# Kernel tuning notes

Measured on AMD Instinct MI355X. Metric: run time of the kernel, lower is better.

Reference implementation:

```python
import jax, jax.numpy as jnp
import numpy as np

B, S, D = 4, 2048, 1024
H = 16
HD = D // H  # 64
ROPE_BASE = 10000.0


def _rope_cache(seq_len, dim, dtype=jnp.float32):
    inv_freq = 1.0 / (ROPE_BASE ** (jnp.arange(0, dim, 2, dtype=jnp.float32) / dim))
    t = jnp.arange(seq_len, dtype=jnp.float32)
    freqs = jnp.outer(t, inv_freq)            # [S, dim/2]
    emb = jnp.concatenate([freqs, freqs], -1)  # [S, dim]
    return jnp.cos(emb).astype(dtype), jnp.sin(emb).astype(dtype)


def _rotate_half(x):
    x1, x2 = jnp.split(x, 2, axis=-1)
    return jnp.concatenate([-x2, x1], axis=-1)


def setup_inputs() -> dict:
    key = jax.random.key(0)
    k1, k2, k3 = jax.random.split(key, 3)
    x = jax.random.normal(k1, (B, S, D), dtype=jnp.float32)
    attention_mask = jnp.ones((B, S), dtype=jnp.int32)
    # torch nn.Linear weight is [out, in]; we store [in, out] for x @ W
    w_qkv = jax.random.normal(k2, (D, 3 * D), dtype=jnp.float32) * (1.0 / np.sqrt(D))
    w_out = jax.random.normal(k3, (D, D), dtype=jnp.float32) * (1.0 / np.sqrt(D))
    return {"x": x, "attention_mask": attention_mask, "w_qkv": w_qkv, "w_out": w_out}


def reference(x, attention_mask, w_qkv, w_out):
    b, s, d = x.shape
    qkv = x @ w_qkv                                  # [B,S,3D]
    qkv = qkv.reshape(b, s, 3, H, HD)
    q, k, v = [jnp.transpose(qkv[:, :, i], (0, 2, 1, 3)) for i in range(3)]  # [B,H,S,HD]
    cos, sin = _rope_cache(s, HD, x.dtype)           # [S,HD]
    cos = cos[None, None]                            # [1,1,S,HD]
    sin = sin[None, None]
    q = q * cos + _rotate_half(q) * sin
    k = k * cos + _rotate_half(k) * sin
    scale = 1.0 / np.sqrt(HD)
    scores = jnp.einsum("bhqd,bhkd->bhqk", q, k) * scale  # [B,H,S,S]
    causal = jnp.triu(jnp.ones((s, s), dtype=bool), k=1)
    neg_inf = jnp.finfo(scores.dtype).min
    scores = jnp.where(causal[None, None], -jnp.inf, scores)
    pad = (attention_mask == 0)[:, None, None, :]    # [B,1,1,S]
    scores = jnp.where(pad, -jnp.inf, scores)
    attn = jax.nn.softmax(scores, axis=-1)
    out = jnp.einsum("bhqk,bhkd->bhqd", attn, v)     # [B,H,S,HD]
    out = jnp.transpose(out, (0, 2, 1, 3)).reshape(b, s, d)
    return out @ w_out
```

## Files before the change

### kernel.cpp

```cpp
#include <hip/hip_runtime.h>

#define BQ 4
#define SQ 2048
#define DQ 1024
#define HQ 16
#define BHQ 64

typedef __attribute__((ext_vector_type(8))) short short8;
typedef __attribute__((ext_vector_type(4))) float f32x4;
typedef __attribute__((ext_vector_type(16))) float f32x16;
typedef __attribute__((ext_vector_type(2))) unsigned int u32x2;
typedef unsigned short u16;
typedef unsigned int u32;
typedef unsigned long long u64;

__device__ __forceinline__ u16 f2bf(float f) {
  u32 u = __float_as_uint(f);
  u32 r = u + 0x7fffu + ((u >> 16) & 1u);
  return (u16)(r >> 16);
}
__device__ __forceinline__ float bf2f(u16 h) {
  return __uint_as_float(((u32)h) << 16);
}

__device__ __forceinline__ u32 pkbf(float lo, float hi_) {
  u32 r;
  asm("v_cvt_pk_bf16_f32 %0, %1, %2" : "=v"(r) : "v"(lo), "v"(hi_));
  return r;
}
__device__ __forceinline__ float fexp2(float x) {
  float r;
  asm("v_exp_f32 %0, %1" : "=v"(r) : "v"(x));
  return r;
}
__device__ __forceinline__ float xmax32(float x) { return fmaxf(x, __shfl_xor(x, 32)); }
__device__ __forceinline__ float xsum32(float x) { return x + __shfl_xor(x, 32); }
__device__ __forceinline__ u32 xword(u32 send) { return (u32)__shfl_xor((int)send, 32); }

__device__ __forceinline__ void gload_lds16(const void* g, void* l) {
  __builtin_amdgcn_global_load_lds(
      (const __attribute__((address_space(1))) u32*)(unsigned long long)g,
      (__attribute__((address_space(3))) u32*)(u32)(unsigned long long)l,
      16, 0, 0);
}

__global__ __launch_bounds__(256) void k_cvt(const float* __restrict__ in, u16* __restrict__ out, int n4) {
  int i = blockIdx.x * 256 + threadIdx.x;
  if (i < n4) {
    float4 v = ((const float4*)in)[i];
    ushort4 o;
    o.x = f2bf(v.x); o.y = f2bf(v.y); o.z = f2bf(v.z); o.w = f2bf(v.w);
    ((ushort4*)out)[i] = o;
  }
}

__global__ __launch_bounds__(256) void k_transpose_cvt(const float* __restrict__ in, u16* __restrict__ out,
                                                       int R, int C) {
  __shared__ float t[32][33];
  int c0 = blockIdx.x * 32, r0 = blockIdx.y * 32;
  int tx = threadIdx.x & 31, ty = threadIdx.x >> 5;
  for (int rr = ty; rr < 32; rr += 8)
    t[rr][tx] = in[(size_t)(r0 + rr) * C + c0 + tx];
  __syncthreads();
  for (int rr = ty; rr < 32; rr += 8)
    out[(size_t)(c0 + rr) * R + r0 + tx] = f2bf(t[tx][rr]);
}

__global__ __launch_bounds__(256) void k_rope_table(float* __restrict__ tab) {
  int i = blockIdx.x * 256 + threadIdx.x;
  if (i >= SQ * 32) return;
  int s = i >> 5, dp = i & 31;
  float invf = expf(-0.28782313662425576f * (float)dp);
  float ang = (float)s * invf;
  tab[i * 2] = cosf(ang);
  tab[i * 2 + 1] = sinf(ang);
}

__global__ __launch_bounds__(256) void k_mflags(const int* __restrict__ mask, u64* __restrict__ mbits) {
  int tid = threadIdx.x;
  int b = tid >> 6, c = tid & 63;
  int all1 = 1;
  for (int i = 0; i < 32; ++i) all1 &= (mask[b * SQ + c * 32 + i] != 0) ? 1 : 0;
  u64 m = __ballot(all1);
  if (c == 0) mbits[b] = m;
}

template <int EPI>
__global__ __launch_bounds__(256) void k_gemm(const u16* __restrict__ A, const u16* __restrict__ Bt,
                                              float* __restrict__ Cf, u16* __restrict__ qb,
                                              u16* __restrict__ kb, u16* __restrict__ vTs,
                                              const float* __restrict__ tab, int K) {
  __shared__ u16 lA[128 * 64];
  __shared__ u16 lB[128 * 64];
  int tid = threadIdx.x, w = tid >> 6, l = tid & 63;
  int wm = w >> 1, wn = w & 1;
  int tm = blockIdx.x, tn = blockIdx.y;
  int li = l & 15, lg = l >> 4;
  const u16* gA = A + (size_t)tm * 128 * K;
  const u16* gB = Bt + (size_t)tn * 128 * K;
  f32x4 acc[4][4];
#pragma unroll
  for (int i = 0; i < 4; i++)
#pragma unroll
    for (int j = 0; j < 4; j++) acc[i][j] = (f32x4){0.f, 0.f, 0.f, 0.f};

  int lr = l >> 3, lslot = l & 7;
  int scol = ((lslot ^ lr) * 8);

  for (int kt = 0; kt < K; kt += 64) {
    __syncthreads();
#pragma unroll
    for (int i = 0; i < 4; ++i) {
      int ch = i * 4 + w;
      int row = ch * 8 + lr;
      gload_lds16(gA + (size_t)row * K + kt + scol, &lA[ch * 512]);
      gload_lds16(gB + (size_t)row * K + kt + scol, &lB[ch * 512]);
    }
    __syncthreads();
#pragma unroll
    for (int kk = 0; kk < 2; ++kk) {
      short8 af[4], bfr[4];
#pragma unroll
      for (int mf = 0; mf < 4; ++mf) {
        int row = wm * 64 + mf * 16 + li;
        af[mf] = *(const short8*)&lA[row * 64 + (((kk * 4 + lg)) ^ (row & 7)) * 8];
      }
#pragma unroll
      for (int nf = 0; nf < 4; ++nf) {
        int row = wn * 64 + nf * 16 + li;
        bfr[nf] = *(const short8*)&lB[row * 64 + (((kk * 4 + lg)) ^ (row & 7)) * 8];
      }
#pragma unroll
      for (int mf = 0; mf < 4; ++mf)
#pragma unroll
        for (int nf = 0; nf < 4; ++nf)
          acc[mf][nf] = __builtin_amdgcn_mfma_f32_16x16x32_bf16(af[mf], bfr[nf], acc[mf][nf], 0, 0, 0);
    }
  }
  if (EPI == 0) {
#pragma unroll
    for (int mf = 0; mf < 4; ++mf) {
      int mg0 = tm * 128 + wm * 64 + mf * 16 + lg * 4;
#pragma unroll
      for (int nf = 0; nf < 4; ++nf) {
        int ng = tn * 128 + wn * 64 + nf * 16 + li;
#pragma unroll
        for (int r = 0; r < 4; ++r)
          Cf[(size_t)(mg0 + r) * 1024 + ng] = acc[mf][nf][r];
      }
    }
  } else {
    int which = tn >> 3;
    int h = (tn & 7) * 2 + wn;
    int b = tm >> 4;
    if (which < 2) {
      float scale = (which == 0) ? 0.125f * 1.44269504088896f : 1.0f;
      u16* qk = (which == 0 ? qb : kb) + (((size_t)b * HQ + h) * SQ << 6);
#pragma unroll
      for (int mf = 0; mf < 4; ++mf) {
#pragma unroll
        for (int r = 0; r < 4; ++r) {
          int s = (tm * 128 + wm * 64 + mf * 16 + lg * 4 + r) & 2047;
          u16* dst = qk + ((size_t)s << 6);
#pragma unroll
          for (int nf2 = 0; nf2 < 2; ++nf2) {
            int dp = nf2 * 16 + li;
            float2 cs = *(const float2*)&tab[(s * 32 + dp) * 2];
            float a = acc[mf][nf2][r];
            float bb = acc[mf][nf2 + 2][r];
            dst[dp] = f2bf((a * cs.x - bb * cs.y) * scale);
            dst[dp + 32] = f2bf((bb * cs.x + a * cs.y) * scale);
          }
        }
      }
    } else {
#pragma unroll
      for (int mf = 0; mf < 4; ++mf) {
        int s0 = (tm * 128 + wm * 64 + mf * 16 + lg * 4) & 2047;
        int kt = s0 >> 5, kk0 = s0 & 31;
        int slot = kk0 >> 3;
        size_t tb = (((size_t)(b * HQ + h) * 64 + kt) * 64);
#pragma unroll
        for (int nf = 0; nf < 4; ++nf) {
          int d = nf * 16 + li;
          u32 w0 = pkbf(acc[mf][nf][0], acc[mf][nf][1]);
          u32 w1 = pkbf(acc[mf][nf][2], acc[mf][nf][3]);
          size_t off = (tb + d) * 32 + ((slot ^ ((d >> 1) & 3)) << 3) + (kk0 & 7);
          *(u32x2*)&vTs[off] = (u32x2){w0, w1};
        }
      }
    }
  }
}

__global__ __launch_bounds__(256) void k_flash7(const u16* __restrict__ Q, const u16* __restrict__ Kb,
                                                const u16* __restrict__ VTs, const int* __restrict__ mask,
                                                const u64* __restrict__ mbits, u16* __restrict__ O) {
  __shared__ alignas(16) u16 Kl[2][2048];
  __shared__ alignas(16) u16 Vl[2][2048];
  int bid = blockIdx.x;
  int bh = bid & 63;
  int u = bid >> 6, v = u & 3, k4 = u >> 2;
  int qsup = (k4 == 0) ? v : (k4 == 1) ? 7 - v : (k4 == 2) ? 8 + v : 15 - v;
  int tid = threadIdx.x, w = tid >> 6, l = tid & 63;
  int j = l & 31, hi = l >> 5;
  int myqt = qsup * 4 + w;
  int nt = qsup * 4 + 4;
  int b = bh >> 4, h = bh & 15;
  const int* mp = mask + b * SQ + 4 * hi;
  u64 mb = mbits[b];

  int sr = tid >> 3, sc16 = tid & 7;
  const u16* Kg0 = Kb + ((size_t)bh * SQ) * 64 + sr * 64 + ((sc16 ^ (sr & 7)) * 8);
  const u16* Vg0 = VTs + ((size_t)bh * 64) * 2048 + tid * 8;
  u16* KlB = &Kl[0][(size_t)w * 512];
  u16* VlB = &Vl[0][(size_t)w * 512];

  int qbase = myqt * 32;
  const u16* qp = Q + ((size_t)bh * SQ + qbase + j) * 64 + hi * 8;
  short8 qf[4];
#pragma unroll
  for (int kb = 0; kb < 4; ++kb) qf[kb] = *(const short8*)(qp + kb * 16);

  f32x16 o0, o1;
#pragma unroll
  for (int i = 0; i < 16; ++i) { o0[i] = 0.f; o1[i] = 0.f; }
  float mrun = -INFINITY, lrun = 0.f;

  int swK = (j & 7), swV = (j >> 1) & 3;

  gload_lds16(Kg0, KlB);
  gload_lds16(Vg0, VlB);
  __syncthreads();

  for (int kt = 0; kt < nt; ++kt) {
    int cur = kt & 1;
    if (kt + 1 < nt) {
      gload_lds16(Kg0 + (size_t)(kt + 1) * 2048, KlB + (cur ^ 1) * 2048);
      gload_lds16(Vg0 + (size_t)(kt + 1) * 2048, VlB + (cur ^ 1) * 2048);
    }

    if (kt <= myqt) {
      const u16* Kc = Kl[cur];
      const u16* Vc = Vl[cur];

      short8 kcf[4];
#pragma unroll
      for (int kb = 0; kb < 4; ++kb)
        kcf[kb] = *(const short8*)&Kc[j * 64 + (((hi + 2 * kb)) ^ swK) * 8];

      f32x16 s;
#pragma unroll
      for (int i = 0; i < 16; ++i) s[i] = 0.f;
      __builtin_amdgcn_s_setprio(1);
#pragma unroll
      for (int kb = 0; kb < 4; ++kb)
        s = __builtin_amdgcn_mfma_f32_32x32x16_bf16(kcf[kb], qf[kb], s, 0, 0, 0);
      __builtin_amdgcn_s_setprio(0);

      short8 va0 = *(const short8*)&Vc[j * 32 + ((hi) ^ swV) * 8];
      short8 va1 = *(const short8*)&Vc[j * 32 + ((hi + 2) ^ swV) * 8];
      short8 vb0 = *(const short8*)&Vc[(j + 32) * 32 + ((hi) ^ swV) * 8];
      short8 vb1 = *(const short8*)&Vc[(j + 32) * 32 + ((hi + 2) ^ swV) * 8];

      if (!((mb >> kt) & 1ull)) {
#pragma unroll
        for (int rq = 0; rq < 4; ++rq) {
          int4 mv = *(const int4*)(mp + kt * 32 + 8 * rq);
          if (!mv.x) s[4 * rq + 0] = -INFINITY;
          if (!mv.y) s[4 * rq + 1] = -INFINITY;
          if (!mv.z) s[4 * rq + 2] = -INFINITY;
          if (!mv.w) s[4 * rq + 3] = -INFINITY;
        }
      }
      if (kt == myqt) {
#pragma unroll
        for (int rq = 0; rq < 4; ++rq)
#pragma unroll
          for (int t = 0; t < 4; ++t)
            if (8 * rq + 4 * hi + t > j) s[4 * rq + t] = -INFINITY;
      }

      float t0 = fmaxf(fmaxf(fmaxf(s[0], s[1]), fmaxf(s[2], s[3])),
                       fmaxf(fmaxf(s[4], s[5]), fmaxf(s[6], s[7])));
      t0 = fmaxf(t0, fmaxf(fmaxf(fmaxf(s[8], s[9]), fmaxf(s[10], s[11])),
                           fmaxf(fmaxf(s[12], s[13]), fmaxf(s[14], s[15]))));
      if (!__all(t0 <= mrun + 8.0f)) {
        float tm2 = xmax32(t0);
        float mn = fmaxf(fmaxf(mrun, tm2), -1e30f);
        float alpha = fexp2(mrun - mn);
        mrun = mn;
        lrun *= alpha;
#pragma unroll
        for (int i = 0; i < 16; ++i) { o0[i] *= alpha; o1[i] *= alpha; }
      }
      float ts = 0.f;
#pragma unroll
      for (int i = 0; i < 16; ++i) {
        float pv = fexp2(s[i] - mrun);
        s[i] = pv;
        ts += pv;
      }
      lrun += ts;

      u32 pa[4], pb[4];
#pragma unroll
      for (int q2 = 0; q2 < 4; ++q2) {
        pa[q2] = pkbf(s[4 * q2 + 0], s[4 * q2 + 1]);
        pb[q2] = pkbf(s[4 * q2 + 2], s[4 * q2 + 3]);
      }
      u32 ya01 = xword(hi ? pa[0] : pa[1]);
      u32 yb01 = xword(hi ? pb[0] : pb[1]);
      u32 ya23 = xword(hi ? pa[2] : pa[3]);
      u32 yb23 = xword(hi ? pb[2] : pb[3]);
      union { short8 s8; u32 wd[4]; } f0, f1;
      f0.wd[0] = hi ? ya01 : pa[0];
      f0.wd[1] = hi ? yb01 : pb[0];
      f0.wd[2] = hi ? pa[1] : ya01;
      f0.wd[3] = hi ? pb[1] : yb01;
      f1.wd[0] = hi ? ya23 : pa[2];
      f1.wd[1] = hi ? yb23 : pb[2];
      f1.wd[2] = hi ? pa[3] : ya23;
      f1.wd[3] = hi ? pb[3] : yb23;

      __builtin_amdgcn_s_setprio(1);
      o0 = __builtin_amdgcn_mfma_f32_32x32x16_bf16(va0, f0.s8, o0, 0, 0, 0);
      o0 = __builtin_amdgcn_mfma_f32_32x32x16_bf16(va1, f1.s8, o0, 0, 0, 0);
      o1 = __builtin_amdgcn_mfma_f32_32x32x16_bf16(vb0, f0.s8, o1, 0, 0, 0);
      o1 = __builtin_amdgcn_mfma_f32_32x32x16_bf16(vb1, f1.s8, o1, 0, 0, 0);
      __builtin_amdgcn_s_setprio(0);
    }

    __syncthreads();
  }

  float lfull = xsum32(lrun);
  float inv = 1.0f / lfull;
  u16* ob = O + ((size_t)b * SQ + qbase + j) * DQ + h * 64 + 4 * hi;
#pragma unroll
  for (int q2 = 0; q2 < 4; ++q2) {
#pragma unroll
    for (int e = 0; e < 2; ++e) {
      *(u32*)(ob + 8 * q2 + 2 * e) = pkbf(o0[4 * q2 + 2 * e] * inv, o0[4 * q2 + 2 * e + 1] * inv);
      *(u32*)(ob + 32 + 8 * q2 + 2 * e) = pkbf(o1[4 * q2 + 2 * e] * inv, o1[4 * q2 + 2 * e + 1] * inv);
    }
  }
}

extern "C" void kernel_launch(void* const* d_in, const int* in_sizes, int n_in,
                              void* d_out, int out_size, void* d_ws, size_t ws_size,
                              hipStream_t stream) {
  const float* x = (const float*)d_in[0];
  const int* mask = (const int*)d_in[1];
  const float* wqkv = (const float*)d_in[2];
  const float* wout = (const float*)d_in[3];
  float* out = (float*)d_out;
  char* ws = (char*)d_ws;

  u16* xb    = (u16*)(ws + 0);
  u16* wqkvT = (u16*)(ws + 16777216);
  u16* woutT = (u16*)(ws + 23068672);
  u16* qbuf  = (u16*)(ws + 25165824);
  u16* kbuf  = (u16*)(ws + 41943040);
  u16* vTs   = (u16*)(ws + 75497472);
  u16* attnb = (u16*)(ws + 92274688);
  float* tab = (float*)(ws + 109051904);
  u64* mbits = (u64*)(ws + 109576192);

  k_rope_table<<<256, 256, 0, stream>>>(tab);
  k_mflags<<<1, 256, 0, stream>>>(mask, mbits);
  k_cvt<<<8192, 256, 0, stream>>>(x, xb, 2097152);
  k_transpose_cvt<<<dim3(96, 32), 256, 0, stream>>>(wqkv, wqkvT, 1024, 3072);
  k_transpose_cvt<<<dim3(32, 32), 256, 0, stream>>>(wout, woutT, 1024, 1024);
  k_gemm<1><<<dim3(64, 24), 256, 0, stream>>>(xb, wqkvT, nullptr, qbuf, kbuf, vTs, tab, 1024);
  k_flash7<<<1024, 256, 0, stream>>>(qbuf, kbuf, vTs, mask, mbits, attnb);
  k_gemm<0><<<dim3(64, 8), 256, 0, stream>>>(attnb, woutT, out, nullptr, nullptr, nullptr, nullptr, 1024);
}
```

Measured before the change: 198.2 us.

## Fuse preprocessing kernels into one launch and swizzle GEMM block mapping for XCD locality

```diff
diff --git a/kernel.cpp b/kernel.cpp
--- a/kernel.cpp
+++ b/kernel.cpp
@@ -44,21 +44,11 @@
       16, 0, 0);
 }
 
-__global__ __launch_bounds__(256) void k_cvt(const float* __restrict__ in, u16* __restrict__ out, int n4) {
-  int i = blockIdx.x * 256 + threadIdx.x;
-  if (i < n4) {
-    float4 v = ((const float4*)in)[i];
-    ushort4 o;
-    o.x = f2bf(v.x); o.y = f2bf(v.y); o.z = f2bf(v.z); o.w = f2bf(v.w);
-    ((ushort4*)out)[i] = o;
-  }
-}
-
-__global__ __launch_bounds__(256) void k_transpose_cvt(const float* __restrict__ in, u16* __restrict__ out,
-                                                       int R, int C) {
+__device__ __forceinline__ void transpose_body(const float* __restrict__ in, u16* __restrict__ out,
+                                               int R, int C, int bx, int by, int tid) {
   __shared__ float t[32][33];
-  int c0 = blockIdx.x * 32, r0 = blockIdx.y * 32;
-  int tx = threadIdx.x & 31, ty = threadIdx.x >> 5;
+  int c0 = bx * 32, r0 = by * 32;
+  int tx = tid & 31, ty = tid >> 5;
   for (int rr = ty; rr < 32; rr += 8)
     t[rr][tx] = in[(size_t)(r0 + rr) * C + c0 + tx];
   __syncthreads();
@@ -66,23 +56,38 @@
     out[(size_t)(c0 + rr) * R + r0 + tx] = f2bf(t[tx][rr]);
 }
 
-__global__ __launch_bounds__(256) void k_rope_table(float* __restrict__ tab) {
-  int i = blockIdx.x * 256 + threadIdx.x;
-  if (i >= SQ * 32) return;
-  int s = i >> 5, dp = i & 31;
-  float invf = expf(-0.28782313662425576f * (float)dp);
-  float ang = (float)s * invf;
-  tab[i * 2] = cosf(ang);
-  tab[i * 2 + 1] = sinf(ang);
-}
-
-__global__ __launch_bounds__(256) void k_mflags(const int* __restrict__ mask, u64* __restrict__ mbits) {
-  int tid = threadIdx.x;
-  int b = tid >> 6, c = tid & 63;
-  int all1 = 1;
-  for (int i = 0; i < 32; ++i) all1 &= (mask[b * SQ + c * 32 + i] != 0) ? 1 : 0;
-  u64 m = __ballot(all1);
-  if (c == 0) mbits[b] = m;
+__global__ __launch_bounds__(256) void k_prep(const float* __restrict__ x, u16* __restrict__ xb,
+                                              const float* __restrict__ wqkv, u16* __restrict__ wqkvT,
+                                              const float* __restrict__ wout, u16* __restrict__ woutT,
+                                              float* __restrict__ tab, const int* __restrict__ mask,
+                                              u64* __restrict__ mbits) {
+  int bid = blockIdx.x, tid = threadIdx.x;
+  if (bid < 8192) {
+    int i = bid * 256 + tid;
+    float4 v = ((const float4*)x)[i];
+    ushort4 o;
+    o.x = f2bf(v.x); o.y = f2bf(v.y); o.z = f2bf(v.z); o.w = f2bf(v.w);
+    ((ushort4*)xb)[i] = o;
+  } else if (bid < 11264) {
+    int t = bid - 8192;
+    transpose_body(wqkv, wqkvT, 1024, 3072, t % 96, t / 96, tid);
+  } else if (bid < 12288) {
+    int t = bid - 11264;
+    transpose_body(wout, woutT, 1024, 1024, t % 32, t / 32, tid);
+  } else if (bid < 12544) {
+    int i = (bid - 12288) * 256 + tid;
+    int s = i >> 5, dp = i & 31;
+    float invf = expf(-0.28782313662425576f * (float)dp);
+    float ang = (float)s * invf;
+    tab[i * 2] = cosf(ang);
+    tab[i * 2 + 1] = sinf(ang);
+  } else {
+    int b = tid >> 6, c = tid & 63;
+    int all1 = 1;
+    for (int i = 0; i < 32; ++i) all1 &= (mask[b * SQ + c * 32 + i] != 0) ? 1 : 0;
+    u64 m = __ballot(all1);
+    if (c == 0) mbits[b] = m;
+  }
 }
 
 template <int EPI>
@@ -92,9 +97,12 @@
                                               const float* __restrict__ tab, int K) {
   __shared__ u16 lA[128 * 64];
   __shared__ u16 lB[128 * 64];
+  int bid = blockIdx.x;
+  int i_ = bid >> 3;
+  int tm = (bid & 7) * 8 + (i_ & 7);
+  int tn = i_ >> 3;
   int tid = threadIdx.x, w = tid >> 6, l = tid & 63;
   int wm = w >> 1, wn = w & 1;
-  int tm = blockIdx.x, tn = blockIdx.y;
   int li = l & 15, lg = l >> 4;
   const u16* gA = A + (size_t)tm * 128 * K;
   const u16* gB = Bt + (size_t)tn * 128 * K;
@@ -367,12 +375,8 @@
   float* tab = (float*)(ws + 109051904);
   u64* mbits = (u64*)(ws + 109576192);
 
-  k_rope_table<<<256, 256, 0, stream>>>(tab);
-  k_mflags<<<1, 256, 0, stream>>>(mask, mbits);
-  k_cvt<<<8192, 256, 0, stream>>>(x, xb, 2097152);
-  k_transpose_cvt<<<dim3(96, 32), 256, 0, stream>>>(wqkv, wqkvT, 1024, 3072);
-  k_transpose_cvt<<<dim3(32, 32), 256, 0, stream>>>(wout, woutT, 1024, 1024);
-  k_gemm<1><<<dim3(64, 24), 256, 0, stream>>>(xb, wqkvT, nullptr, qbuf, kbuf, vTs, tab, 1024);
+  k_prep<<<12545, 256, 0, stream>>>(x, xb, wqkv, wqkvT, wout, woutT, tab, mask, mbits);
+  k_gemm<1><<<1536, 256, 0, stream>>>(xb, wqkvT, nullptr, qbuf, kbuf, vTs, tab, 1024);
   k_flash7<<<1024, 256, 0, stream>>>(qbuf, kbuf, vTs, mask, mbits, attnb);
-  k_gemm<0><<<dim3(64, 8), 256, 0, stream>>>(attnb, woutT, out, nullptr, nullptr, nullptr, nullptr, 1024);
-}
+  k_gemm<0><<<512, 256, 0, stream>>>(attnb, woutT, out, nullptr, nullptr, nullptr, nullptr, 1024);
+}
```

Measured after the change: 188.0 us. 5.2% less time.
